# Kernel optimization log

Measured on AMD Instinct MI355X. Metric: run time of the kernel, lower is better.

Reference implementation:

```python
import math
import jax, jax.numpy as jnp
import numpy as np

B, Q, L, H = 32, 40, 1024, 1024
WINDOW_FRAMES, MAX_V_L = 16, 1024
MAX_DELTA = 0.1
NUM_PASSES = 2


def setup_inputs() -> dict:
    key = jax.random.key(0)
    ks = jax.random.split(key, 8)
    init_log_sigma = math.log(WINDOW_FRAMES / (2.0 * MAX_V_L))
    return {
        "pred_spans": jax.random.uniform(ks[0], (B, Q, 2), dtype=jnp.float32),
        "vid_feat": jax.random.normal(ks[1], (B, L, H), dtype=jnp.float32),
        "vid_mask": jnp.ones((B, L), dtype=jnp.float32),
        "txt_rep": jax.random.normal(ks[2], (B, H), dtype=jnp.float32),
        "log_sigma_start": jnp.float32(init_log_sigma),
        "log_sigma_end": jnp.float32(init_log_sigma),
        "sigma_width_scale_start": jnp.float32(0.01),
        "sigma_width_scale_end": jnp.float32(-0.01),
        "txt_proj_w": jax.random.normal(ks[3], (H, 2), dtype=jnp.float32) * 0.02,
        "txt_proj_b": jnp.zeros((2,), dtype=jnp.float32),
        "mlp0_w": jax.random.normal(ks[4], (3 * H, H), dtype=jnp.float32) * (1.0 / math.sqrt(3 * H)),
        "mlp0_b": jnp.zeros((H,), dtype=jnp.float32),
        "mlp1_w": jax.random.normal(ks[5], (H, 2), dtype=jnp.float32) * (1.0 / math.sqrt(H)),
        "mlp1_b": jnp.zeros((2,), dtype=jnp.float32),
    }


def reference(pred_spans, vid_feat, vid_mask, txt_rep,
              log_sigma_start, log_sigma_end,
              sigma_width_scale_start, sigma_width_scale_end,
              txt_proj_w, txt_proj_b, mlp0_w, mlp0_b, mlp1_w, mlp1_b):
    b, q, _ = pred_spans.shape
    l = vid_feat.shape[1]
    # span (center,width) -> (start,end) in [0,1]
    start = jnp.clip(pred_spans[..., 0] - pred_spans[..., 1] / 2, 0.0, 1.0)  # (B,Q)
    end = jnp.clip(pred_spans[..., 0] + pred_spans[..., 1] / 2, 0.0, 1.0)
    t_pos = jnp.linspace(0.0, 1.0, l)  # (L,)
    min_sig = 1.0 / (4.0 * l)
    log_range = math.log(max(float(l) * min_sig * 4.0, 1.0 + 1e-6))
    # semantic sigma offsets (B,2)
    txt_off = jnp.tanh(txt_rep @ txt_proj_w + txt_proj_b) * (0.5 * log_range)
    txt_off_s, txt_off_e = txt_off[:, 0:1], txt_off[:, 1:2]  # (B,1)
    txt_expand = jnp.broadcast_to(txt_rep[:, None, :], (b, q, txt_rep.shape[-1]))
    mask = vid_mask[:, None, :]  # (B,1,L)

    def _pool(anchor, sigma):
        # Gaussian soft-attention pooling over frames; anchor,sigma: (B,Q)
        dist2 = ((t_pos[None, None, :] - anchor[:, :, None]) / sigma[:, :, None]) ** 2
        w = jnp.exp(-0.5 * dist2) * mask  # (B,Q,L)
        w = w / jnp.maximum(jnp.sum(w, -1, keepdims=True), 1e-8)
        return jnp.einsum('bql,blh->bqh', w, vid_feat)

    passes = []
    for _ in range(NUM_PASSES):
        width = jnp.maximum(end - start, 1e-6)  # (B,Q)
        sig_s = jnp.maximum(jnp.exp(log_sigma_start + sigma_width_scale_start * width + txt_off_s), min_sig)
        sig_e = jnp.maximum(jnp.exp(log_sigma_end + sigma_width_scale_end * width + txt_off_e), min_sig)
        start_feat = _pool(start, sig_s)
        end_feat = _pool(end, sig_e)
        joint = jnp.concatenate([start_feat, end_feat, txt_expand], axis=-1)  # (B,Q,3H)
        hidden = jax.nn.relu(joint @ mlp0_w + mlp0_b)
        deltas = jnp.tanh(hidden @ mlp1_w + mlp1_b) * MAX_DELTA  # (B,Q,2)
        start = jnp.clip(start + deltas[..., 0], 0.0, 1.0)
        end = jnp.clip(end + deltas[..., 1], 0.0, 1.0)
        center_r = (start + end) / 2.0
        width_r = jnp.maximum(end - start, 1e-6)
        passes.append(jnp.stack([center_r, width_r], axis=-1))
    return passes[-1], jnp.stack(passes, axis=0)
```

## Files before the change

kernel.cpp:

```cpp
#include <hip/hip_runtime.h>

#define B_   32
#define Q_   40
#define L_   1024
#define H_   1024
#define QQ_  80
#define M_   1280
#define K3_  3072
#define JK_  2048

#define OB_VIDT  0u
#define OB_W0T   67108864u
#define OB_WT2   73400320u
#define OB_JOINT 78643200u
#define OB_PART  83886080u
#define OB_TXTB  94371840u
#define OB_TXTP  94437376u
#define OB_MISC  94699520u
#define MS_START 0
#define MS_END   1280
#define MS_TOS   2560
#define MS_TOE   2592

typedef short bf8 __attribute__((ext_vector_type(8)));
typedef float f4  __attribute__((ext_vector_type(4)));

static __device__ __forceinline__ unsigned short f2b(float f) {
    unsigned int x = __float_as_uint(f);
    unsigned int r = x + 0x7FFFu + ((x >> 16) & 1u);
    return (unsigned short)(r >> 16);
}
static __device__ __forceinline__ float b2f16(unsigned short u) {
    return __uint_as_float((unsigned int)u << 16);
}
static __device__ __forceinline__ float blo(unsigned int u) {
    return __uint_as_float(u << 16);
}
static __device__ __forceinline__ float bhi(unsigned int u) {
    return __uint_as_float(u & 0xffff0000u);
}

__global__ __launch_bounds__(256) void k_setup(const float* __restrict__ vid,
                                               unsigned short* __restrict__ vidT,
                                               const float* __restrict__ w0,
                                               unsigned short* __restrict__ w0t,
                                               const float* __restrict__ txt,
                                               const float* __restrict__ pw,
                                               const float* __restrict__ pb,
                                               const float* __restrict__ spans,
                                               unsigned short* __restrict__ txtb,
                                               float* __restrict__ msc) {
    int z = blockIdx.z, tid = threadIdx.x;
    if (z == 35) {
        int flat = blockIdx.x * 16 + blockIdx.y;
        if (flat < B_) {
            int b = flat;
            int h4 = tid * 4;
            float4 tv = *(const float4*)(txt + (size_t)b * H_ + h4);
            float4 pa = *(const float4*)(pw + 2 * h4);
            float4 pc = *(const float4*)(pw + 2 * h4 + 4);
            float s0 = tv.x * pa.x + tv.y * pa.z + tv.z * pc.x + tv.w * pc.z;
            float s1 = tv.x * pa.y + tv.y * pa.w + tv.z * pc.y + tv.w * pc.w;
            ushort4 o;
            o.x = f2b(tv.x); o.y = f2b(tv.y); o.z = f2b(tv.z); o.w = f2b(tv.w);
            *(ushort4*)(txtb + (size_t)b * H_ + h4) = o;
            __shared__ float r0[256], r1[256];
            r0[tid] = s0; r1[tid] = s1; __syncthreads();
            for (int off = 128; off > 0; off >>= 1) {
                if (tid < off) { r0[tid] += r0[tid + off]; r1[tid] += r1[tid + off]; }
                __syncthreads();
            }
            if (tid == 0) {
                const float half_lr = 4.9999975e-07f;
                msc[MS_TOS + b] = tanhf(r0[0] + pb[0]) * half_lr;
                msc[MS_TOE + b] = tanhf(r1[0] + pb[1]) * half_lr;
            }
        } else if (flat < 37) {
            int i = (flat - B_) * 256 + tid;
            if (i < M_) {
                float c = spans[2 * i], w = spans[2 * i + 1];
                msc[MS_START + i] = fminf(fmaxf(c - 0.5f * w, 0.f), 1.f);
                msc[MS_END + i]   = fminf(fmaxf(c + 0.5f * w, 0.f), 1.f);
            }
        }
        return;
    }
    __shared__ float tile[64][69];
    const float* s;
    unsigned short* d;
    int dstRowStride;
    if (z < B_) {
        s = vid + (size_t)z * L_ * H_;
        d = vidT + (size_t)z * H_ * L_;
        dstRowStride = L_;
    } else {
        int zz = z - B_;
        s = w0 + (size_t)zz * 1024 * H_;
        d = w0t + (size_t)zz * 1024;
        dstRowStride = K3_;
    }
    int r0 = blockIdx.x * 64, c0 = blockIdx.y * 64;
    int col4 = (tid & 15) * 4, row = tid >> 4;
    #pragma unroll
    for (int it = 0; it < 4; it++) {
        int r = it * 16 + row;
        float4 v = *(const float4*)(s + (size_t)(r0 + r) * 1024 + c0 + col4);
        *(float4*)(&tile[r][col4]) = v;
    }
    __syncthreads();
    #pragma unroll
    for (int it = 0; it < 2; it++) {
        int slot = it * 256 + tid;
        int c = slot >> 3, chunk = slot & 7;
        int r = chunk * 8;
        uint4 vv;
        vv.x = (unsigned int)f2b(tile[r + 0][c]) | ((unsigned int)f2b(tile[r + 1][c]) << 16);
        vv.y = (unsigned int)f2b(tile[r + 2][c]) | ((unsigned int)f2b(tile[r + 3][c]) << 16);
        vv.z = (unsigned int)f2b(tile[r + 4][c]) | ((unsigned int)f2b(tile[r + 5][c]) << 16);
        vv.w = (unsigned int)f2b(tile[r + 6][c]) | ((unsigned int)f2b(tile[r + 7][c]) << 16);
        *(uint4*)(d + (size_t)(c0 + c) * dstRowStride + r0 + r) = vv;
    }
}

static __device__ __forceinline__ void weights_body(int m, float s, float e,
                                                    const float* __restrict__ vmask,
                                                    float ls_s, float ls_e,
                                                    float sw_s, float sw_e,
                                                    const float* __restrict__ msc,
                                                    unsigned short* __restrict__ wt2,
                                                    float* r0, float* r1) {
    int b = m / Q_, q = m - b * Q_;
    int tid = threadIdx.x;
    float width = fmaxf(e - s, 1e-6f);
    const float min_sig = 1.0f / (4.0f * (float)L_);
    float sig_s = fmaxf(expf(ls_s + sw_s * width + msc[MS_TOS + b]), min_sig);
    float sig_e = fmaxf(expf(ls_e + sw_e * width + msc[MS_TOE + b]), min_sig);
    float inv_s = 1.0f / sig_s, inv_e = 1.0f / sig_e;

    float wsv[4], wev[4], sumS = 0.f, sumE = 0.f;
    #pragma unroll
    for (int k = 0; k < 4; k++) {
        int l = tid + k * 256;
        float t = (float)l * (1.0f / 1023.0f);
        float mk = vmask[b * L_ + l];
        float ds = (t - s) * inv_s, de = (t - e) * inv_e;
        float a = expf(-0.5f * ds * ds) * mk;
        float c = expf(-0.5f * de * de) * mk;
        wsv[k] = a; wev[k] = c; sumS += a; sumE += c;
    }
    r0[tid] = sumS; r1[tid] = sumE; __syncthreads();
    for (int off = 128; off > 0; off >>= 1) {
        if (tid < off) { r0[tid] += r0[tid + off]; r1[tid] += r1[tid + off]; }
        __syncthreads();
    }
    float iS = 1.0f / fmaxf(r0[0], 1e-8f);
    float iE = 1.0f / fmaxf(r1[0], 1e-8f);
    unsigned short* wq = wt2 + ((size_t)b * QQ_ + q) * L_;
    unsigned short* we = wt2 + ((size_t)b * QQ_ + Q_ + q) * L_;
    #pragma unroll
    for (int k = 0; k < 4; k++) {
        int l = tid + k * 256;
        wq[l] = f2b(wsv[k] * iS);
        we[l] = f2b(wev[k] * iE);
    }
}

__global__ __launch_bounds__(256) void k_stage2(const float* __restrict__ vmask,
                                                const float* __restrict__ p_ls_s,
                                                const float* __restrict__ p_ls_e,
                                                const float* __restrict__ p_sw_s,
                                                const float* __restrict__ p_sw_e,
                                                const float* __restrict__ msc,
                                                unsigned short* __restrict__ wt2,
                                                const unsigned short* __restrict__ txtb,
                                                const unsigned short* __restrict__ w0t,
                                                unsigned short* __restrict__ txtp) {
    int bid = blockIdx.x;
    if (bid < M_) {
        __shared__ float r0[256], r1[256];
        int m = bid;
        weights_body(m, msc[MS_START + m], msc[MS_END + m], vmask,
                     p_ls_s[0], p_ls_e[0], p_sw_s[0], p_sw_e[0], msc, wt2, r0, r1);
        return;
    }
    int t = bid - M_;
    int nIdx = t & 15, mIdx = (t >> 4) & 1, kIdx = t >> 5;
    int wv = threadIdx.x >> 6, lane = threadIdx.x & 63;
    int ml = lane & 15, kg = lane >> 4;
    int mbase = mIdx * 16;
    int nbase = nIdx * 64 + wv * 16;
    int kz = kIdx * 256;
    const unsigned short* ap = txtb + ((size_t)(mbase + ml) * H_ + kz + kg * 8);
    const unsigned short* bp = w0t + ((size_t)(nbase + ml) * K3_ + JK_ + kz + kg * 8);
    f4 acc = (f4){0.f, 0.f, 0.f, 0.f};
    #pragma unroll
    for (int k0 = 0; k0 < 256; k0 += 32) {
        bf8 a = *(const bf8*)(ap + k0);
        bf8 bb = *(const bf8*)(bp + k0);
        acc = __builtin_amdgcn_mfma_f32_16x16x32_bf16(a, bb, acc, 0, 0, 0);
    }
    unsigned short* pp = txtp + (size_t)kIdx * B_ * H_;
    int n = nbase + ml;
    #pragma unroll
    for (int r = 0; r < 4; r++) {
        int m = mbase + kg * 4 + r;
        pp[(size_t)m * H_ + n] = f2b(acc[r]);
    }
}

__global__ __launch_bounds__(512) void k_pool_mfma(const unsigned short* __restrict__ vidT,
                                                   const unsigned short* __restrict__ wt2,
                                                   unsigned short* __restrict__ joint) {
    int b = blockIdx.x, ht = blockIdx.y;
    int wv = threadIdx.x >> 6, lane = threadIdx.x & 63;
    int hsub = wv & 3, half = wv >> 2;
    int ml = lane & 15, kg = lane >> 4;
    int hbase = ht * 64 + hsub * 16;
    const unsigned short* ap = vidT + (((size_t)b * H_ + hbase + ml) * L_ + half * 512 + kg * 8);
    const unsigned short* bp = wt2 + (((size_t)b * QQ_ + ml) * L_ + half * 512 + kg * 8);
    f4 acc[5];
    #pragma unroll
    for (int t = 0; t < 5; t++) acc[t] = (f4){0.f, 0.f, 0.f, 0.f};

    #pragma unroll 4
    for (int l0 = 0; l0 < 512; l0 += 32) {
        bf8 a = *(const bf8*)(ap + l0);
        #pragma unroll
        for (int t = 0; t < 5; t++) {
            bf8 bb = *(const bf8*)(bp + (size_t)t * 16 * L_ + l0);
            acc[t] = __builtin_amdgcn_mfma_f32_16x16x32_bf16(a, bb, acc[t], 0, 0, 0);
        }
    }

    __shared__ float cmb[4][5][64][4];
    if (half == 1) {
        #pragma unroll
        for (int t = 0; t < 5; t++) {
            *(f4*)(&cmb[hsub][t][lane][0]) = acc[t];
        }
    }
    __syncthreads();
    if (half == 0) {
        #pragma unroll
        for (int t = 0; t < 5; t++) {
            f4 o = *(const f4*)(&cmb[hsub][t][lane][0]);
            acc[t] += o;
            int qq = t * 16 + ml;
            int row = b * Q_ + (qq >= Q_ ? qq - Q_ : qq);
            int col = (qq >= Q_ ? H_ : 0) + hbase + kg * 4;
            ushort4 v;
            v.x = f2b(acc[t][0]); v.y = f2b(acc[t][1]);
            v.z = f2b(acc[t][2]); v.w = f2b(acc[t][3]);
            *(ushort4*)(joint + (size_t)row * JK_ + col) = v;
        }
    }
}

__global__ __launch_bounds__(256) void k_mlp0_mfma(const unsigned short* __restrict__ joint,
                                                   const unsigned short* __restrict__ w0t,
                                                   const unsigned short* __restrict__ txtp,
                                                   unsigned short* __restrict__ part) {
    int wv = threadIdx.x >> 6, lane = threadIdx.x & 63;
    int ml = lane & 15, kg = lane >> 4;
    int mbase = blockIdx.x * 64 + wv * 16;
    int nbase = blockIdx.y * 64;
    int kbase = blockIdx.z * 512;
    const unsigned short* ap = joint + ((size_t)(mbase + ml) * JK_ + kbase + kg * 8);
    const unsigned short* bp = w0t + ((size_t)(nbase + ml) * K3_ + kbase + kg * 8);
    f4 acc[4];
    #pragma unroll
    for (int t = 0; t < 4; t++) acc[t] = (f4){0.f, 0.f, 0.f, 0.f};

    #pragma unroll 4
    for (int k0 = 0; k0 < 512; k0 += 32) {
        bf8 a = *(const bf8*)(ap + k0);
        #pragma unroll
        for (int t = 0; t < 4; t++) {
            bf8 bb = *(const bf8*)(bp + (size_t)t * 16 * K3_ + k0);
            acc[t] = __builtin_amdgcn_mfma_f32_16x16x32_bf16(a, bb, acc[t], 0, 0, 0);
        }
    }
    const unsigned short* tp = txtp + (size_t)blockIdx.z * B_ * H_;
    unsigned short* pp = part + (size_t)blockIdx.z * M_ * H_;
    #pragma unroll
    for (int t = 0; t < 4; t++) {
        int n = nbase + t * 16 + ml;
        #pragma unroll
        for (int r = 0; r < 4; r++) {
            int m = mbase + kg * 4 + r;
            int b = m / Q_;
            float v = acc[t][r] + b2f16(tp[(size_t)b * H_ + n]);
            pp[(size_t)m * H_ + n] = f2b(v);
        }
    }
}

__global__ __launch_bounds__(256) void k_mlp1w(const float* __restrict__ w1,
                                               const float* __restrict__ b0,
                                               const float* __restrict__ b1,
                                               const unsigned short* __restrict__ part,
                                               float* __restrict__ msc,
                                               float* __restrict__ out, int pass,
                                               int do_weights,
                                               const float* __restrict__ vmask,
                                               const float* __restrict__ p_ls_s,
                                               const float* __restrict__ p_ls_e,
                                               const float* __restrict__ p_sw_s,
                                               const float* __restrict__ p_sw_e,
                                               unsigned short* __restrict__ wt2) {
    int m = blockIdx.x, tid = threadIdx.x;
    int k4 = tid * 4;
    float4 bb = *(const float4*)(b0 + k4);
    float h0 = bb.x, h1 = bb.y, h2 = bb.z, h3 = bb.w;
    #pragma unroll
    for (int z = 0; z < 4; z++) {
        uint2 u = *(const uint2*)(part + (size_t)z * M_ * H_ + (size_t)m * H_ + k4);
        h0 += blo(u.x); h1 += bhi(u.x);
        h2 += blo(u.y); h3 += bhi(u.y);
    }
    h0 = fmaxf(h0, 0.f); h1 = fmaxf(h1, 0.f);
    h2 = fmaxf(h2, 0.f); h3 = fmaxf(h3, 0.f);
    float4 wa = *(const float4*)(w1 + 2 * k4);
    float4 wb = *(const float4*)(w1 + 2 * k4 + 4);
    float p0 = h0 * wa.x + h1 * wa.z + h2 * wb.x + h3 * wb.z;
    float p1 = h0 * wa.y + h1 * wa.w + h2 * wb.y + h3 * wb.w;

    __shared__ float r0[256], r1[256];
    __shared__ float sh_s, sh_e;
    r0[tid] = p0; r1[tid] = p1; __syncthreads();
    for (int off = 128; off > 0; off >>= 1) {
        if (tid < off) { r0[tid] += r0[tid + off]; r1[tid] += r1[tid + off]; }
        __syncthreads();
    }
    if (tid == 0) {
        float d0 = tanhf(r0[0] + b1[0]) * 0.1f;
        float d1 = tanhf(r1[0] + b1[1]) * 0.1f;
        float s = fminf(fmaxf(msc[MS_START + m] + d0, 0.f), 1.f);
        float e = fminf(fmaxf(msc[MS_END + m] + d1, 0.f), 1.f);
        msc[MS_START + m] = s;
        msc[MS_END + m] = e;
        sh_s = s; sh_e = e;
        float cen = 0.5f * (s + e);
        float wid = fmaxf(e - s, 1e-6f);
        out[2560 + (size_t)(pass * M_ + m) * 2 + 0] = cen;
        out[2560 + (size_t)(pass * M_ + m) * 2 + 1] = wid;
        if (pass == 1) { out[2 * m + 0] = cen; out[2 * m + 1] = wid; }
    }
    __syncthreads();
    if (do_weights) {
        weights_body(m, sh_s, sh_e, vmask,
                     p_ls_s[0], p_ls_e[0], p_sw_s[0], p_sw_e[0], msc, wt2, r0, r1);
    }
}

extern "C" void kernel_launch(void* const* d_in, const int* in_sizes, int n_in,
                              void* d_out, int out_size, void* d_ws, size_t ws_size,
                              hipStream_t stream) {
    const float* spans = (const float*)d_in[0];
    const float* vid   = (const float*)d_in[1];
    const float* vmask = (const float*)d_in[2];
    const float* txt   = (const float*)d_in[3];
    const float* ls_s  = (const float*)d_in[4];
    const float* ls_e  = (const float*)d_in[5];
    const float* sw_s  = (const float*)d_in[6];
    const float* sw_e  = (const float*)d_in[7];
    const float* pw    = (const float*)d_in[8];
    const float* pb    = (const float*)d_in[9];
    const float* w0    = (const float*)d_in[10];
    const float* b0    = (const float*)d_in[11];
    const float* w1    = (const float*)d_in[12];
    const float* b1    = (const float*)d_in[13];
    char* wsb = (char*)d_ws;
    unsigned short* vidT  = (unsigned short*)(wsb + OB_VIDT);
    unsigned short* w0t   = (unsigned short*)(wsb + OB_W0T);
    unsigned short* wt2   = (unsigned short*)(wsb + OB_WT2);
    unsigned short* joint = (unsigned short*)(wsb + OB_JOINT);
    unsigned short* part  = (unsigned short*)(wsb + OB_PART);
    unsigned short* txtb  = (unsigned short*)(wsb + OB_TXTB);
    unsigned short* txtp  = (unsigned short*)(wsb + OB_TXTP);
    float* msc = (float*)(wsb + OB_MISC);
    float* out = (float*)d_out;

    hipLaunchKernelGGL(k_setup, dim3(16, 16, 36), dim3(256), 0, stream,
                       vid, vidT, w0, w0t, txt, pw, pb, spans, txtb, msc);
    hipLaunchKernelGGL(k_stage2, dim3(M_ + 128), dim3(256), 0, stream,
                       vmask, ls_s, ls_e, sw_s, sw_e, msc, wt2, txtb, w0t, txtp);
    for (int p = 0; p < 2; p++) {
        hipLaunchKernelGGL(k_pool_mfma, dim3(B_, 16), dim3(512), 0, stream, vidT, wt2, joint);
        hipLaunchKernelGGL(k_mlp0_mfma, dim3(20, 16, 4), dim3(256), 0, stream,
                           joint, w0t, txtp, part);
        hipLaunchKernelGGL(k_mlp1w, dim3(M_), dim3(256), 0, stream,
                           w1, b0, b1, part, msc, out, p, (p == 0) ? 1 : 0,
                           vmask, ls_s, ls_e, sw_s, sw_e, wt2);
    }
}
```

Baseline: 435.5 us.

## Fuse video transpose and bf16 conversion into pooling kernel via LDS staging

Removes the separate pass that transposed the fp32 video features into a bf16 copy in workspace. The pooling kernel now reads fp32 video rows directly, converts them to bf16 and transposes them through double-buffered shared memory tiles before the MFMA. This avoids writing and re-reading a 64 MB intermediate. In exchange, each of the two pooling passes reads the fp32 video (twice the bytes of bf16) and adds scalar LDS stores and a barrier per chunk.

```diff
diff --git a/kernel.cpp b/kernel.cpp
--- a/kernel.cpp
+++ b/kernel.cpp
@@ -9,14 +9,13 @@
 #define K3_  3072
 #define JK_  2048
 
-#define OB_VIDT  0u
-#define OB_W0T   67108864u
-#define OB_WT2   73400320u
-#define OB_JOINT 78643200u
-#define OB_PART  83886080u
-#define OB_TXTB  94371840u
-#define OB_TXTP  94437376u
-#define OB_MISC  94699520u
+#define OB_W0T   0u
+#define OB_WT2   6291456u
+#define OB_JOINT 11534336u
+#define OB_PART  16777216u
+#define OB_TXTB  27262976u
+#define OB_TXTP  27328512u
+#define OB_MISC  27590656u
 #define MS_START 0
 #define MS_END   1280
 #define MS_TOS   2560
@@ -40,9 +39,7 @@
     return __uint_as_float(u & 0xffff0000u);
 }
 
-__global__ __launch_bounds__(256) void k_setup(const float* __restrict__ vid,
-                                               unsigned short* __restrict__ vidT,
-                                               const float* __restrict__ w0,
+__global__ __launch_bounds__(256) void k_setup(const float* __restrict__ w0,
                                                unsigned short* __restrict__ w0t,
                                                const float* __restrict__ txt,
                                                const float* __restrict__ pw,
@@ -51,7 +48,7 @@
                                                unsigned short* __restrict__ txtb,
                                                float* __restrict__ msc) {
     int z = blockIdx.z, tid = threadIdx.x;
-    if (z == 35) {
+    if (z == 3) {
         int flat = blockIdx.x * 16 + blockIdx.y;
         if (flat < B_) {
             int b = flat;
@@ -86,19 +83,8 @@
         return;
     }
     __shared__ float tile[64][69];
-    const float* s;
-    unsigned short* d;
-    int dstRowStride;
-    if (z < B_) {
-        s = vid + (size_t)z * L_ * H_;
-        d = vidT + (size_t)z * H_ * L_;
-        dstRowStride = L_;
-    } else {
-        int zz = z - B_;
-        s = w0 + (size_t)zz * 1024 * H_;
-        d = w0t + (size_t)zz * 1024;
-        dstRowStride = K3_;
-    }
+    const float* s = w0 + (size_t)z * 1024 * H_;
+    unsigned short* d = w0t + (size_t)z * 1024;
     int r0 = blockIdx.x * 64, c0 = blockIdx.y * 64;
     int col4 = (tid & 15) * 4, row = tid >> 4;
     #pragma unroll
@@ -118,7 +104,7 @@
         vv.y = (unsigned int)f2b(tile[r + 2][c]) | ((unsigned int)f2b(tile[r + 3][c]) << 16);
         vv.z = (unsigned int)f2b(tile[r + 4][c]) | ((unsigned int)f2b(tile[r + 5][c]) << 16);
         vv.w = (unsigned int)f2b(tile[r + 6][c]) | ((unsigned int)f2b(tile[r + 7][c]) << 16);
-        *(uint4*)(d + (size_t)(c0 + c) * dstRowStride + r0 + r) = vv;
+        *(uint4*)(d + (size_t)(c0 + c) * K3_ + r0 + r) = vv;
     }
 }
 
@@ -208,51 +194,99 @@
     }
 }
 
-__global__ __launch_bounds__(512) void k_pool_mfma(const unsigned short* __restrict__ vidT,
+__global__ __launch_bounds__(512) void k_pool_mfma(const float* __restrict__ vid,
                                                    const unsigned short* __restrict__ wt2,
                                                    unsigned short* __restrict__ joint) {
     int b = blockIdx.x, ht = blockIdx.y;
-    int wv = threadIdx.x >> 6, lane = threadIdx.x & 63;
+    int tid = threadIdx.x;
+    int wv = tid >> 6, lane = tid & 63;
     int hsub = wv & 3, half = wv >> 2;
     int ml = lane & 15, kg = lane >> 4;
-    int hbase = ht * 64 + hsub * 16;
-    const unsigned short* ap = vidT + (((size_t)b * H_ + hbase + ml) * L_ + half * 512 + kg * 8);
-    const unsigned short* bp = wt2 + (((size_t)b * QQ_ + ml) * L_ + half * 512 + kg * 8);
+    int h0 = ht * 64;
+
+    __shared__ __align__(16) unsigned short tileT[2][2][64][40];
+    __shared__ float cmb[80][68];
+
+    int st = tid & 255;
+    int sl = st >> 3;
+    int sh8 = (st & 7) * 8;
+    const float* vbase = vid + ((size_t)b * L_ + half * 512) * H_ + h0;
+
+    const unsigned short* ap = wt2 + ((size_t)b * QQ_ + ml) * L_ + half * 512 + kg * 8;
+
     f4 acc[5];
     #pragma unroll
     for (int t = 0; t < 5; t++) acc[t] = (f4){0.f, 0.f, 0.f, 0.f};
 
-    #pragma unroll 4
-    for (int l0 = 0; l0 < 512; l0 += 32) {
-        bf8 a = *(const bf8*)(ap + l0);
+    {
+        const float* src = vbase + (size_t)sl * H_ + sh8;
+        float4 v0 = *(const float4*)(src);
+        float4 v1 = *(const float4*)(src + 4);
+        unsigned short* dst = &tileT[half][0][0][0];
+        dst[(sh8 + 0) * 40 + sl] = f2b(v0.x);
+        dst[(sh8 + 1) * 40 + sl] = f2b(v0.y);
+        dst[(sh8 + 2) * 40 + sl] = f2b(v0.z);
+        dst[(sh8 + 3) * 40 + sl] = f2b(v0.w);
+        dst[(sh8 + 4) * 40 + sl] = f2b(v1.x);
+        dst[(sh8 + 5) * 40 + sl] = f2b(v1.y);
+        dst[(sh8 + 6) * 40 + sl] = f2b(v1.z);
+        dst[(sh8 + 7) * 40 + sl] = f2b(v1.w);
+    }
+    __syncthreads();
+
+    for (int c = 0; c < 16; c++) {
+        int buf = c & 1;
+        if (c < 15) {
+            const float* src = vbase + (size_t)((c + 1) * 32 + sl) * H_ + sh8;
+            float4 v0 = *(const float4*)(src);
+            float4 v1 = *(const float4*)(src + 4);
+            unsigned short* dst = &tileT[half][buf ^ 1][0][0];
+            dst[(sh8 + 0) * 40 + sl] = f2b(v0.x);
+            dst[(sh8 + 1) * 40 + sl] = f2b(v0.y);
+            dst[(sh8 + 2) * 40 + sl] = f2b(v0.z);
+            dst[(sh8 + 3) * 40 + sl] = f2b(v0.w);
+            dst[(sh8 + 4) * 40 + sl] = f2b(v1.x);
+            dst[(sh8 + 5) * 40 + sl] = f2b(v1.y);
+            dst[(sh8 + 6) * 40 + sl] = f2b(v1.z);
+            dst[(sh8 + 7) * 40 + sl] = f2b(v1.w);
+        }
+        bf8 bfrag = *(const bf8*)(&tileT[half][buf][hsub * 16 + ml][kg * 8]);
+        int l0 = c * 32;
         #pragma unroll
         for (int t = 0; t < 5; t++) {
-            bf8 bb = *(const bf8*)(bp + (size_t)t * 16 * L_ + l0);
-            acc[t] = __builtin_amdgcn_mfma_f32_16x16x32_bf16(a, bb, acc[t], 0, 0, 0);
+            bf8 afr = *(const bf8*)(ap + (size_t)t * 16 * L_ + l0);
+            acc[t] = __builtin_amdgcn_mfma_f32_16x16x32_bf16(afr, bfrag, acc[t], 0, 0, 0);
         }
-    }
-
-    __shared__ float cmb[4][5][64][4];
+        __syncthreads();
+    }
+
     if (half == 1) {
         #pragma unroll
-        for (int t = 0; t < 5; t++) {
-            *(f4*)(&cmb[hsub][t][lane][0]) = acc[t];
-        }
+        for (int t = 0; t < 5; t++)
+            #pragma unroll
+            for (int r = 0; r < 4; r++)
+                cmb[t * 16 + kg * 4 + r][hsub * 16 + ml] = acc[t][r];
     }
     __syncthreads();
     if (half == 0) {
         #pragma unroll
-        for (int t = 0; t < 5; t++) {
-            f4 o = *(const f4*)(&cmb[hsub][t][lane][0]);
-            acc[t] += o;
-            int qq = t * 16 + ml;
-            int row = b * Q_ + (qq >= Q_ ? qq - Q_ : qq);
-            int col = (qq >= Q_ ? H_ : 0) + hbase + kg * 4;
-            ushort4 v;
-            v.x = f2b(acc[t][0]); v.y = f2b(acc[t][1]);
-            v.z = f2b(acc[t][2]); v.w = f2b(acc[t][3]);
-            *(ushort4*)(joint + (size_t)row * JK_ + col) = v;
-        }
+        for (int t = 0; t < 5; t++)
+            #pragma unroll
+            for (int r = 0; r < 4; r++)
+                cmb[t * 16 + kg * 4 + r][hsub * 16 + ml] += acc[t][r];
+    }
+    __syncthreads();
+    for (int idx = tid; idx < 640; idx += 512) {
+        int qq = idx >> 3, h8 = (idx & 7) * 8;
+        const float* cr = &cmb[qq][h8];
+        uint4 vv;
+        vv.x = (unsigned int)f2b(cr[0]) | ((unsigned int)f2b(cr[1]) << 16);
+        vv.y = (unsigned int)f2b(cr[2]) | ((unsigned int)f2b(cr[3]) << 16);
+        vv.z = (unsigned int)f2b(cr[4]) | ((unsigned int)f2b(cr[5]) << 16);
+        vv.w = (unsigned int)f2b(cr[6]) | ((unsigned int)f2b(cr[7]) << 16);
+        int row = b * Q_ + (qq >= Q_ ? qq - Q_ : qq);
+        int col = (qq >= Q_ ? H_ : 0) + h0 + h8;
+        *(uint4*)(joint + (size_t)row * JK_ + col) = vv;
     }
 }
 
@@ -371,7 +405,6 @@
     const float* w1    = (const float*)d_in[12];
     const float* b1    = (const float*)d_in[13];
     char* wsb = (char*)d_ws;
-    unsigned short* vidT  = (unsigned short*)(wsb + OB_VIDT);
     unsigned short* w0t   = (unsigned short*)(wsb + OB_W0T);
     unsigned short* wt2   = (unsigned short*)(wsb + OB_WT2);
     unsigned short* joint = (unsigned short*)(wsb + OB_JOINT);
@@ -381,12 +414,12 @@
     float* msc = (float*)(wsb + OB_MISC);
     float* out = (float*)d_out;
 
-    hipLaunchKernelGGL(k_setup, dim3(16, 16, 36), dim3(256), 0, stream,
-                       vid, vidT, w0, w0t, txt, pw, pb, spans, txtb, msc);
+    hipLaunchKernelGGL(k_setup, dim3(16, 16, 4), dim3(256), 0, stream,
+                       w0, w0t, txt, pw, pb, spans, txtb, msc);
     hipLaunchKernelGGL(k_stage2, dim3(M_ + 128), dim3(256), 0, stream,
                        vmask, ls_s, ls_e, sw_s, sw_e, msc, wt2, txtb, w0t, txtp);
     for (int p = 0; p < 2; p++) {
-        hipLaunchKernelGGL(k_pool_mfma, dim3(B_, 16), dim3(512), 0, stream, vidT, wt2, joint);
+        hipLaunchKernelGGL(k_pool_mfma, dim3(B_, 16), dim3(512), 0, stream, vid, wt2, joint);
         hipLaunchKernelGGL(k_mlp0_mfma, dim3(20, 16, 4), dim3(256), 0, stream,
                            joint, w0t, txtp, part);
         hipLaunchKernelGGL(k_mlp1w, dim3(M_), dim3(256), 0, stream,
```

New measurement: 396.9 us. 1.1x faster.
